# Optimization experiments

Measured on AMD Instinct MI355X. Metric: run time of the kernel, lower is better.

Reference implementation:

```python
import jax, jax.numpy as jnp
import numpy as np

B, T, C, H = 4, 2048, 768, 12
D = C // H  # head dim = 64
EPS = 1e-5


def setup_inputs() -> dict:
    key = jax.random.key(0)
    ks = jax.random.split(key, 12)
    s = lambda fan_in: 1.0 / np.sqrt(fan_in)
    return {
        "x": jax.random.normal(ks[0], (B, T, C), dtype=jnp.float32),
        "ln1_g": jnp.ones((C,), jnp.float32),
        "ln1_b": jnp.zeros((C,), jnp.float32),
        "w_attn": jax.random.normal(ks[1], (C, 3 * C), jnp.float32) * s(C),
        "b_attn": jnp.zeros((3 * C,), jnp.float32),
        "w_aproj": jax.random.normal(ks[2], (C, C), jnp.float32) * s(C),
        "b_aproj": jnp.zeros((C,), jnp.float32),
        "ln2_g": jnp.ones((C,), jnp.float32),
        "ln2_b": jnp.zeros((C,), jnp.float32),
        "w_fc": jax.random.normal(ks[3], (C, 4 * C), jnp.float32) * s(C),
        "b_fc": jnp.zeros((4 * C,), jnp.float32),
        "w_mproj": jax.random.normal(ks[4], (4 * C, C), jnp.float32) * s(4 * C),
        "b_mproj": jnp.zeros((C,), jnp.float32),
    }


def _layernorm(x, g, b):
    mu = jnp.mean(x, axis=-1, keepdims=True)
    var = jnp.mean(jnp.square(x - mu), axis=-1, keepdims=True)
    return (x - mu) * jax.lax.rsqrt(var + EPS) * g + b


def _attention(h, w_attn, b_attn, w_aproj, b_aproj):
    qkv = h @ w_attn + b_attn                          # [B,T,3C]
    q, k, v = jnp.split(qkv, 3, axis=-1)
    q = q.reshape(B, T, H, D)
    k = k.reshape(B, T, H, D)
    v = v.reshape(B, T, H, D)
    att = jnp.einsum("bqhd,bkhd->bhqk", q, k) * (1.0 / np.sqrt(D))
    causal = jnp.tril(jnp.ones((T, T), bool))
    att = jnp.where(causal, att, -jnp.inf)
    att = jax.nn.softmax(att, axis=-1)
    y = jnp.einsum("bhqk,bkhd->bqhd", att, v).reshape(B, T, C)
    return y @ w_aproj + b_aproj


def reference(x, ln1_g, ln1_b, w_attn, b_attn, w_aproj, b_aproj,
              ln2_g, ln2_b, w_fc, b_fc, w_mproj, b_mproj):
    x = x + _attention(_layernorm(x, ln1_g, ln1_b), w_attn, b_attn, w_aproj, b_aproj)
    h = _layernorm(x, ln2_g, ln2_b)
    h = jax.nn.gelu(h @ w_fc + b_fc, approximate=True)  # tanh approximation, matches F.gelu(approximate='tanh')
    x = x + (h @ w_mproj + b_mproj)
    return x
```

## Files before the change

### kernel.cpp

```cpp
#include <hip/hip_runtime.h>


typedef unsigned short ushortT;
typedef unsigned int uintT;
typedef __attribute__((ext_vector_type(8))) __bf16 bf16x8;
typedef __attribute__((ext_vector_type(4))) float f32x4;

#define MFMA16(a, b, c) __builtin_amdgcn_mfma_f32_16x16x32_bf16(a, b, c, 0, 0, 0)

__device__ inline float b2f(ushortT u) {
  return __uint_as_float(((uintT)u) << 16);
}
__device__ inline ushortT f2b(float f) {
  uintT x = __float_as_uint(f);
  uintT r = x + 0x7fffu + ((x >> 16) & 1u);
  return (ushortT)(r >> 16);
}
__device__ inline uintT pack_bf2(float a, float b) {
  return __builtin_amdgcn_perm(__float_as_uint(b), __float_as_uint(a),
                               0x07060302u);
}

__device__ inline float gelu_tanh(float v) {
  float t = 0.7978845608028654f * (v + 0.044715f * v * v * v);
  return v / (1.0f + __expf(-2.0f * t));
}

__device__ __forceinline__ void glds16(const ushortT* g, ushortT* l) {
  __builtin_amdgcn_global_load_lds(
      (const __attribute__((address_space(1))) unsigned int*)(const void*)g,
      (__attribute__((address_space(3))) unsigned int*)(void*)l, 16, 0, 0);
}

__global__ __launch_bounds__(256) void detect_dtype(
    const ushortT* __restrict__ w, int* __restrict__ flag) {
  __shared__ int red;
  if (threadIdx.x == 0) red = 0;
  __syncthreads();
  int crazy = 0;
  for (int i = threadIdx.x; i < 4096; i += 256) {
    uintT e = (w[2 * i] >> 7) & 0xFF;
    if (e >= 150) crazy = 1;
  }
  if (crazy) atomicOr(&red, 1);
  __syncthreads();
  if (threadIdx.x == 0) *flag = red;
}

struct VecArgs {
  const void* src[8];
  int n[8];
  int dstoff[8];
};
__global__ __launch_bounds__(256) void convert_vecs(
    VecArgs a, ushortT* __restrict__ pv, const int* __restrict__ flag) {
  int fl = *flag;
  int t = blockIdx.y;
  int i = blockIdx.x * 256 + threadIdx.x;
  if (i >= a.n[t]) return;
  float v = fl ? ((const float*)a.src[t])[i] : b2f(((const ushortT*)a.src[t])[i]);
  pv[a.dstoff[t] + i] = f2b(v);
}

__global__ __launch_bounds__(256) void transpose_any(
    const void* __restrict__ in, ushortT* __restrict__ out, int K, int N,
    const int* __restrict__ flag) {
  __shared__ ushortT t[32][33];
  int fl = *flag;
  int n0 = blockIdx.x * 32, k0 = blockIdx.y * 32;
  int x = threadIdx.x, y0 = threadIdx.y;
#pragma unroll
  for (int i = y0; i < 32; i += 8) {
    size_t idx = (size_t)(k0 + i) * N + n0 + x;
    t[i][x] = fl ? f2b(((const float*)in)[idx]) : ((const ushortT*)in)[idx];
  }
  __syncthreads();
#pragma unroll
  for (int i = y0; i < 32; i += 8)
    out[(size_t)(n0 + i) * K + k0 + x] = t[x][i];
}

__global__ __launch_bounds__(256) void vtrans_kernel(
    const ushortT* __restrict__ qkv, ushortT* __restrict__ vt) {
  const int T = 2048, C3 = 2304;
  __shared__ ushortT tile[64][65];
  int bh = blockIdx.y;
  int b = bh / 12, h = bh % 12;
  int t0 = blockIdx.x * 64;
  int col = threadIdx.x & 63, rowi = threadIdx.x >> 6;
#pragma unroll
  for (int rr = rowi; rr < 64; rr += 4)
    tile[rr][col] =
        qkv[((size_t)(b * T + t0 + rr)) * C3 + 1536 + h * 64 + col];
  __syncthreads();
#pragma unroll
  for (int dd = rowi; dd < 64; dd += 4)
    vt[((size_t)bh * 64 + dd) * T + t0 + col] = tile[col][dd];
}

template <int MODE>
__global__ __launch_bounds__(256) void ln_kernel(
    const void* __restrict__ xin, const ushortT* __restrict__ g,
    const ushortT* __restrict__ bb, ushortT* __restrict__ out,
    const int* __restrict__ flag) {
  const int C = 768;
  bool f32;
  if constexpr (MODE == 1) f32 = true; else f32 = (*flag != 0);
  size_t base = (size_t)blockIdx.x * C;
  int tid = threadIdx.x;
  const float* xf = (const float*)xin;
  const ushortT* xb = (const ushortT*)xin;
  float v0 = f32 ? xf[base + tid]       : b2f(xb[base + tid]);
  float v1 = f32 ? xf[base + tid + 256] : b2f(xb[base + tid + 256]);
  float v2 = f32 ? xf[base + tid + 512] : b2f(xb[base + tid + 512]);
  float s = v0 + v1 + v2;
  float q = v0 * v0 + v1 * v1 + v2 * v2;
#pragma unroll
  for (int off = 32; off; off >>= 1) {
    s += __shfl_xor(s, off);
    q += __shfl_xor(q, off);
  }
  __shared__ float as_[4], aq_[4];
  if ((tid & 63) == 0) { as_[tid >> 6] = s; aq_[tid >> 6] = q; }
  __syncthreads();
  s = as_[0] + as_[1] + as_[2] + as_[3];
  q = aq_[0] + aq_[1] + aq_[2] + aq_[3];
  float mu = s * (1.0f / 768.0f);
  float var = q * (1.0f / 768.0f) - mu * mu;
  float rs = rsqrtf(var + 1e-5f);
  ushortT* orow = out + base;
  orow[tid]       = f2b((v0 - mu) * rs * b2f(g[tid])       + b2f(bb[tid]));
  orow[tid + 256] = f2b((v1 - mu) * rs * b2f(g[tid + 256]) + b2f(bb[tid + 256]));
  orow[tid + 512] = f2b((v2 - mu) * rs * b2f(g[tid + 512]) + b2f(bb[tid + 512]));
}

template <int EPI>
__global__ __launch_bounds__(512, 2) void gemm_dp(
    const ushortT* __restrict__ A, const ushortT* __restrict__ Bt,
    const ushortT* __restrict__ bias, const void* __restrict__ res,
    void* __restrict__ out, int N, int K, int nbm, int nbn,
    const int* __restrict__ flag) {
  __shared__ ushortT As3[3][128 * 64];
  __shared__ ushortT Bs3[3][256 * 64];
  int fl = (EPI >= 2) ? *flag : 0;
  int tid = threadIdx.x;
  int lane = tid & 63, wave = tid >> 6;
  int quad = lane >> 4, n = lane & 15, n7 = n & 7;
  int mg = wave >> 2, ng = wave & 3;
  int l = blockIdx.x;
  int xcd = l & 7, j = l >> 3;
  int m0 = (xcd * (nbm >> 3) + j / nbn) * 128;
  int n0 = (j % nbn) * 256;

  int trow = tid >> 3;
  int tc = ((tid & 7) ^ (trow & 7)) << 3;
  const ushortT* ga = A + (size_t)(m0 + trow) * K + tc;
  const ushortT* gb = Bt + (size_t)(n0 + trow) * K + tc;
  int lw = wave * 512;

  const int c0 = (quad ^ n7) << 3;
  const int c1 = ((4 + quad) ^ n7) << 3;
  const int arow = (mg * 64 + n) * 64;
  const int brow = (ng * 64 + n) * 64;

  int kt = K >> 6;
  f32x4 acc[4][4] = {};

  auto stage_tile = [&](int tt, int slot) {
    int kk0 = tt << 6;
    ushortT* la = &As3[slot][0] + lw;
    ushortT* lb = &Bs3[slot][0] + lw;
    glds16(ga + kk0, la);
    glds16(ga + (size_t)64 * K + kk0, la + 4096);
    glds16(gb + kk0, lb);
    glds16(gb + (size_t)64 * K + kk0, lb + 4096);
    glds16(gb + (size_t)128 * K + kk0, lb + 8192);
    glds16(gb + (size_t)192 * K + kk0, lb + 12288);
  };

  stage_tile(0, 0);
  stage_tile(1, 1);
  asm volatile("s_waitcnt vmcnt(6)" ::: "memory");
  __builtin_amdgcn_s_barrier();

  int cur = 0;
  for (int t = 0; t < kt; ++t) {
    const ushortT* ca = &As3[cur][0];
    const ushortT* cb = &Bs3[cur][0];
    int nxt = cur + 2; if (nxt >= 3) nxt -= 3;
    bool pf = (t + 2) < kt;
    int pk0 = (t + 2) << 6;
    ushortT* la = &As3[nxt][0] + lw;
    ushortT* lb = &Bs3[nxt][0] + lw;

    bf16x8 af[4][2], bfr[2][2];
#pragma unroll
    for (int mi = 0; mi < 4; ++mi) {
      af[mi][0] = *(const bf16x8*)(ca + arow + mi * 1024 + c0);
      af[mi][1] = *(const bf16x8*)(ca + arow + mi * 1024 + c1);
    }
#pragma unroll
    for (int ni = 0; ni < 2; ++ni) {
      bfr[ni][0] = *(const bf16x8*)(cb + brow + ni * 1024 + c0);
      bfr[ni][1] = *(const bf16x8*)(cb + brow + ni * 1024 + c1);
    }
    if (pf) {
      glds16(ga + pk0, la);
      glds16(ga + (size_t)64 * K + pk0, la + 4096);
      glds16(gb + pk0, lb);
    }
    __builtin_amdgcn_s_barrier();
    __builtin_amdgcn_s_setprio(1);
#pragma unroll
    for (int mi = 0; mi < 4; ++mi)
#pragma unroll
      for (int ni = 0; ni < 2; ++ni) {
        acc[mi][ni] = MFMA16(af[mi][0], bfr[ni][0], acc[mi][ni]);
        acc[mi][ni] = MFMA16(af[mi][1], bfr[ni][1], acc[mi][ni]);
      }
    __builtin_amdgcn_s_setprio(0);
    __builtin_amdgcn_s_barrier();

#pragma unroll
    for (int ni = 0; ni < 2; ++ni) {
      bfr[ni][0] = *(const bf16x8*)(cb + brow + (ni + 2) * 1024 + c0);
      bfr[ni][1] = *(const bf16x8*)(cb + brow + (ni + 2) * 1024 + c1);
    }
    if (pf) {
      glds16(gb + (size_t)64 * K + pk0, lb + 4096);
      glds16(gb + (size_t)128 * K + pk0, lb + 8192);
      glds16(gb + (size_t)192 * K + pk0, lb + 12288);
    }
    __builtin_amdgcn_s_barrier();
    __builtin_amdgcn_s_setprio(1);
#pragma unroll
    for (int mi = 0; mi < 4; ++mi)
#pragma unroll
      for (int ni = 0; ni < 2; ++ni) {
        acc[mi][ni + 2] = MFMA16(af[mi][0], bfr[ni][0], acc[mi][ni + 2]);
        acc[mi][ni + 2] = MFMA16(af[mi][1], bfr[ni][1], acc[mi][ni + 2]);
      }
    __builtin_amdgcn_s_setprio(0);
    if (pf) asm volatile("s_waitcnt vmcnt(6)" ::: "memory");
    else    asm volatile("s_waitcnt vmcnt(0)" ::: "memory");
    __builtin_amdgcn_s_barrier();

    cur = cur + 1; if (cur == 3) cur = 0;
  }

#pragma unroll
  for (int mi = 0; mi < 4; ++mi) {
#pragma unroll
    for (int ni = 0; ni < 4; ++ni) {
      int gc = n0 + ng * 64 + ni * 16 + n;
      float bv = b2f(bias[gc]);
      int gr0 = m0 + mg * 64 + mi * 16 + quad * 4;
#pragma unroll
      for (int r = 0; r < 4; ++r) {
        size_t idx = (size_t)(gr0 + r) * N + gc;
        float v = acc[mi][ni][r] + bv;
        if constexpr (EPI == 1) v = gelu_tanh(v);
        if constexpr (EPI == 2) {
          v += fl ? ((const float*)res)[idx] : b2f(((const ushortT*)res)[idx]);
          ((float*)out)[idx] = v;
        } else if constexpr (EPI == 3) {
          v += ((const float*)res)[idx];
          if (fl) ((float*)out)[idx] = v;
          else    ((ushortT*)out)[idx] = f2b(v);
        } else {
          ((ushortT*)out)[idx] = f2b(v);
        }
      }
    }
  }
}

__global__ __launch_bounds__(256) void attn_kernel(
    const ushortT* __restrict__ qkv, const ushortT* __restrict__ vt,
    ushortT* __restrict__ y) {
  const int T = 2048, C3 = 2304;
  constexpr int LDK = 72, LDP = 72;
  __shared__ ushortT Ks[64 * LDK];
  __shared__ ushortT Vs[64 * LDK];
  __shared__ ushortT Ps[4 * 16 * LDP];
  int bh = blockIdx.y;
  int b = bh / 12, h = bh % 12;
  int pj = blockIdx.x;
  int tid = threadIdx.x;
  int lane = tid & 63, wave = tid >> 6;
  int quad = lane >> 4, n = lane & 15;

  const ushortT* base = qkv + (size_t)b * T * C3;
  const ushortT* kbase = base + 768 + h * 64;
  const ushortT* vbase = vt + (size_t)bh * 64 * T;
  ushortT* myP = Ps + wave * 16 * LDP;

  const float QS = 0.18033688011112042f;
  const float MB = 20.0f;

  int qtA = pj, qtB = 31 - pj;
  int nA = qtA + 1, ntot = 33;

  int trow = tid >> 3, tcol = (tid & 7) << 3;
  const ushortT* kg = kbase + (size_t)trow * C3 + tcol;
  const ushortT* vg = vbase + (size_t)trow * T + tcol;

  int qt = qtA;
  int qw = qt * 64 + wave * 16;
  bf16x8 aq[2];
  {
    const ushortT* qrow = base + (size_t)(qw + n) * C3 + h * 64 + quad * 8;
#pragma unroll
    for (int dh = 0; dh < 2; ++dh) {
      union { ushortT u[8]; bf16x8 v; } tmp;
#pragma unroll
      for (int j = 0; j < 8; ++j) tmp.u[j] = f2b(b2f(qrow[dh * 32 + j]) * QS);
      aq[dh] = tmp.v;
    }
  }
  f32x4 Ot[4] = {};
  float l_ = 0.f;

  uint4 kr0 = *(const uint4*)(kg);
  uint4 kr1 = *(const uint4*)(kg + (size_t)32 * C3);
  uint4 vr0 = *(const uint4*)(vg);
  uint4 vr1 = *(const uint4*)(vg + (size_t)32 * T);

  for (int t = 0; t < ntot; ++t) {
    int kt = (t < nA) ? t : t - nA;
    __syncthreads();
    *(uint4*)(Ks + trow * LDK + tcol) = kr0;
    *(uint4*)(Ks + (trow + 32) * LDK + tcol) = kr1;
    *(uint4*)(Vs + trow * LDK + tcol) = vr0;
    *(uint4*)(Vs + (trow + 32) * LDK + tcol) = vr1;
    __syncthreads();
    if (t + 1 < ntot) {
      int ktn = (t + 1 < nA) ? t + 1 : t + 1 - nA;
      int k0n = ktn << 6;
      kr0 = *(const uint4*)(kg + (size_t)k0n * C3);
      kr1 = *(const uint4*)(kg + (size_t)(k0n + 32) * C3);
      vr0 = *(const uint4*)(vg + k0n);
      vr1 = *(const uint4*)(vg + (size_t)32 * T + k0n);
    }

    f32x4 St[4];
#pragma unroll
    for (int g = 0; g < 4; ++g) {
      bf16x8 ka0 = *(const bf16x8*)(Ks + (g * 16 + n) * LDK + quad * 8);
      bf16x8 ka1 = *(const bf16x8*)(Ks + (g * 16 + n) * LDK + 32 + quad * 8);
      f32x4 z = {};
      z = MFMA16(ka0, aq[0], z);
      St[g] = MFMA16(ka1, aq[1], z);
    }
    if (kt == qt) {
      int lim = wave * 16 + n;
#pragma unroll
      for (int g = 0; g < 4; ++g)
#pragma unroll
        for (int r = 0; r < 4; ++r)
          if (g * 16 + quad * 4 + r > lim) St[g][r] = -1e30f;
    }
    float ls = 0.f;
#pragma unroll
    for (int g = 0; g < 4; ++g) {
      float p0 = exp2f(St[g][0] - MB);
      float p1 = exp2f(St[g][1] - MB);
      float p2 = exp2f(St[g][2] - MB);
      float p3 = exp2f(St[g][3] - MB);
      ls += (p0 + p1) + (p2 + p3);
      uint2 pk;
      pk.x = pack_bf2(p0, p1);
      pk.y = pack_bf2(p2, p3);
      *(uint2*)(myP + n * LDP + g * 16 + quad * 4) = pk;
    }
    ls += __shfl_xor(ls, 16);
    ls += __shfl_xor(ls, 32);
    l_ += ls;

    bf16x8 pb0 = *(const bf16x8*)(myP + n * LDP + quad * 8);
    bf16x8 pb1 = *(const bf16x8*)(myP + n * LDP + 32 + quad * 8);
#pragma unroll
    for (int dt = 0; dt < 4; ++dt) {
      bf16x8 va0 = *(const bf16x8*)(Vs + (dt * 16 + n) * LDK + quad * 8);
      bf16x8 va1 = *(const bf16x8*)(Vs + (dt * 16 + n) * LDK + 32 + quad * 8);
      Ot[dt] = MFMA16(va0, pb0, Ot[dt]);
      Ot[dt] = MFMA16(va1, pb1, Ot[dt]);
    }

    if (kt == qt) {
      float inv = 1.0f / l_;
      int qg = qw + n;
#pragma unroll
      for (int dt = 0; dt < 4; ++dt) {
        uint2 o;
        o.x = pack_bf2(Ot[dt][0] * inv, Ot[dt][1] * inv);
        o.y = pack_bf2(Ot[dt][2] * inv, Ot[dt][3] * inv);
        *(uint2*)(y + (size_t)(b * T + qg) * 768 + h * 64 + dt * 16 +
                  quad * 4) = o;
      }
      if (t + 1 < ntot) {
        qt = qtB;
        qw = qt * 64 + wave * 16;
        const ushortT* qrow =
            base + (size_t)(qw + n) * C3 + h * 64 + quad * 8;
#pragma unroll
        for (int dh = 0; dh < 2; ++dh) {
          union { ushortT u[8]; bf16x8 v; } tmp;
#pragma unroll
          for (int j = 0; j < 8; ++j)
            tmp.u[j] = f2b(b2f(qrow[dh * 32 + j]) * QS);
          aq[dh] = tmp.v;
        }
#pragma unroll
        for (int dt = 0; dt < 4; ++dt)
#pragma unroll
          for (int r = 0; r < 4; ++r) Ot[dt][r] = 0.f;
        l_ = 0.f;
      }
    }
  }
}

extern "C" void kernel_launch(void* const* d_in, const int* in_sizes, int n_in,
                              void* d_out, int out_size, void* d_ws,
                              size_t ws_size, hipStream_t stream) {
  (void)in_sizes; (void)n_in; (void)out_size; (void)ws_size;
  const void* x       = d_in[0];
  const void* w_attn  = d_in[3];
  const void* w_aproj = d_in[5];
  const void* w_fc    = d_in[9];
  const void* w_mproj = d_in[11];

  char* ws = (char*)d_ws;
  ushortT* h1  = (ushortT*)(ws);
  ushortT* qkv = (ushortT*)(ws + 12582912);
  ushortT* yb  = (ushortT*)(ws + 50331648);
  float*   x1  = (float*)(ws + 62914560);
  ushortT* fcg = (ushortT*)(ws + 88080384);
  ushortT* wT0 = (ushortT*)(ws + 138412032);
  ushortT* wT1 = (ushortT*)(ws + 141950976);
  ushortT* wT2 = (ushortT*)(ws + 143130624);
  ushortT* wT3 = (ushortT*)(ws + 147849216);
  ushortT* pv  = (ushortT*)(ws + 152567808);
  int*     flag = (int*)(ws + 152600576);
  ushortT* vt  = h1;
  ushortT* h2  = yb;

  const int O_LN1G = 0, O_LN1B = 768, O_BATT = 1536, O_BAPR = 3840,
            O_LN2G = 4608, O_LN2B = 5376, O_BFC = 6144, O_BMPR = 9216;

  detect_dtype<<<1, 256, 0, stream>>>((const ushortT*)w_fc, flag);

  VecArgs va;
  va.src[0] = d_in[1];  va.n[0] = 768;  va.dstoff[0] = O_LN1G;
  va.src[1] = d_in[2];  va.n[1] = 768;  va.dstoff[1] = O_LN1B;
  va.src[2] = d_in[4];  va.n[2] = 2304; va.dstoff[2] = O_BATT;
  va.src[3] = d_in[6];  va.n[3] = 768;  va.dstoff[3] = O_BAPR;
  va.src[4] = d_in[7];  va.n[4] = 768;  va.dstoff[4] = O_LN2G;
  va.src[5] = d_in[8];  va.n[5] = 768;  va.dstoff[5] = O_LN2B;
  va.src[6] = d_in[10]; va.n[6] = 3072; va.dstoff[6] = O_BFC;
  va.src[7] = d_in[12]; va.n[7] = 768;  va.dstoff[7] = O_BMPR;
  convert_vecs<<<dim3(12, 8), 256, 0, stream>>>(va, pv, flag);

  dim3 tb(32, 8);
  transpose_any<<<dim3(72, 24), tb, 0, stream>>>(w_attn, wT0, 768, 2304, flag);
  transpose_any<<<dim3(24, 24), tb, 0, stream>>>(w_aproj, wT1, 768, 768, flag);
  transpose_any<<<dim3(96, 24), tb, 0, stream>>>(w_fc, wT2, 768, 3072, flag);
  transpose_any<<<dim3(24, 96), tb, 0, stream>>>(w_mproj, wT3, 3072, 768, flag);

  ln_kernel<0><<<8192, 256, 0, stream>>>(x, pv + O_LN1G, pv + O_LN1B, h1, flag);
  gemm_dp<0><<<576, 512, 0, stream>>>(
      h1, wT0, pv + O_BATT, nullptr, qkv, 2304, 768, 64, 9, flag);
  vtrans_kernel<<<dim3(32, 48), 256, 0, stream>>>(qkv, vt);
  attn_kernel<<<dim3(16, 48), 256, 0, stream>>>(qkv, vt, yb);
  gemm_dp<2><<<192, 512, 0, stream>>>(
      yb, wT1, pv + O_BAPR, x, x1, 768, 768, 64, 3, flag);
  ln_kernel<1><<<8192, 256, 0, stream>>>(x1, pv + O_LN2G, pv + O_LN2B, h2, flag);
  gemm_dp<1><<<768, 512, 0, stream>>>(
      h2, wT2, pv + O_BFC, nullptr, fcg, 3072, 768, 64, 12, flag);
  gemm_dp<3><<<192, 512, 0, stream>>>(
      fcg, wT3, pv + O_BMPR, x1, d_out, 768, 3072, 64, 3, flag);
}
```

Before: 419.3 us.

## Double-buffer attention K/V tiles via direct global-to-LDS loads with XOR swizzle

The attention kernel now stages K and V tiles straight into LDS with global_load_lds, using two buffers so the next tile loads while the current one is computed. This removes the register round trip and one of the two barriers per iteration. The padded LDS rows are replaced by an XOR-swizzled 64-wide layout to avoid bank conflicts, and exp2f is swapped for the hardware exp2 builtin. LDS use doubles for K/V, and correctness depends on the swizzle indices on the write and read sides matching.

```diff
diff --git a/kernel.cpp b/kernel.cpp
--- a/kernel.cpp
+++ b/kernel.cpp
@@ -19,6 +19,14 @@
 __device__ inline uintT pack_bf2(float a, float b) {
   return __builtin_amdgcn_perm(__float_as_uint(b), __float_as_uint(a),
                                0x07060302u);
+}
+
+__device__ inline float fast_exp2(float x) {
+#if __has_builtin(__builtin_amdgcn_exp2f)
+  return __builtin_amdgcn_exp2f(x);
+#else
+  return exp2f(x);
+#endif
 }
 
 __device__ inline float gelu_tanh(float v) {
@@ -279,16 +287,16 @@
     const ushortT* __restrict__ qkv, const ushortT* __restrict__ vt,
     ushortT* __restrict__ y) {
   const int T = 2048, C3 = 2304;
-  constexpr int LDK = 72, LDP = 72;
-  __shared__ ushortT Ks[64 * LDK];
-  __shared__ ushortT Vs[64 * LDK];
+  constexpr int LDP = 72;
+  __shared__ ushortT Ks[2][64 * 64];
+  __shared__ ushortT Vs[2][64 * 64];
   __shared__ ushortT Ps[4 * 16 * LDP];
   int bh = blockIdx.y;
   int b = bh / 12, h = bh % 12;
   int pj = blockIdx.x;
   int tid = threadIdx.x;
   int lane = tid & 63, wave = tid >> 6;
-  int quad = lane >> 4, n = lane & 15;
+  int quad = lane >> 4, n = lane & 15, n7 = n & 7;
 
   const ushortT* base = qkv + (size_t)b * T * C3;
   const ushortT* kbase = base + 768 + h * 64;
@@ -301,9 +309,14 @@
   int qtA = pj, qtB = 31 - pj;
   int nA = qtA + 1, ntot = 33;
 
-  int trow = tid >> 3, tcol = (tid & 7) << 3;
-  const ushortT* kg = kbase + (size_t)trow * C3 + tcol;
-  const ushortT* vg = vbase + (size_t)trow * T + tcol;
+  int srow = lane >> 3, scol = lane & 7;
+  const ushortT* kg =
+      kbase + (size_t)(wave * 16 + srow) * C3 + ((scol ^ srow) << 3);
+  const ushortT* vg =
+      vbase + (size_t)(wave * 16 + srow) * T + ((scol ^ srow) << 3);
+
+  const int c0 = (quad ^ n7) << 3;
+  const int c1 = ((4 + quad) ^ n7) << 3;
 
   int qt = qtA;
   int qw = qt * 64 + wave * 16;
@@ -321,33 +334,34 @@
   f32x4 Ot[4] = {};
   float l_ = 0.f;
 
-  uint4 kr0 = *(const uint4*)(kg);
-  uint4 kr1 = *(const uint4*)(kg + (size_t)32 * C3);
-  uint4 vr0 = *(const uint4*)(vg);
-  uint4 vr1 = *(const uint4*)(vg + (size_t)32 * T);
-
+  auto stage = [&](int kt_, int buf) {
+    int kof = kt_ << 6;
+    ushortT* lk = &Ks[buf][0] + wave * 1024;
+    ushortT* lv = &Vs[buf][0] + wave * 1024;
+    glds16(kg + (size_t)kof * C3, lk);
+    glds16(kg + (size_t)(kof + 8) * C3, lk + 512);
+    glds16(vg + kof, lv);
+    glds16(vg + (size_t)8 * T + kof, lv + 512);
+  };
+
+  stage(0, 0);
+  __syncthreads();
+
+  int cur = 0;
   for (int t = 0; t < ntot; ++t) {
     int kt = (t < nA) ? t : t - nA;
-    __syncthreads();
-    *(uint4*)(Ks + trow * LDK + tcol) = kr0;
-    *(uint4*)(Ks + (trow + 32) * LDK + tcol) = kr1;
-    *(uint4*)(Vs + trow * LDK + tcol) = vr0;
-    *(uint4*)(Vs + (trow + 32) * LDK + tcol) = vr1;
-    __syncthreads();
     if (t + 1 < ntot) {
       int ktn = (t + 1 < nA) ? t + 1 : t + 1 - nA;
-      int k0n = ktn << 6;
-      kr0 = *(const uint4*)(kg + (size_t)k0n * C3);
-      kr1 = *(const uint4*)(kg + (size_t)(k0n + 32) * C3);
-      vr0 = *(const uint4*)(vg + k0n);
-      vr1 = *(const uint4*)(vg + (size_t)32 * T + k0n);
-    }
+      stage(ktn, cur ^ 1);
+    }
+    const ushortT* ks = &Ks[cur][0];
+    const ushortT* vs = &Vs[cur][0];
 
     f32x4 St[4];
 #pragma unroll
     for (int g = 0; g < 4; ++g) {
-      bf16x8 ka0 = *(const bf16x8*)(Ks + (g * 16 + n) * LDK + quad * 8);
-      bf16x8 ka1 = *(const bf16x8*)(Ks + (g * 16 + n) * LDK + 32 + quad * 8);
+      bf16x8 ka0 = *(const bf16x8*)(ks + (g * 16 + n) * 64 + c0);
+      bf16x8 ka1 = *(const bf16x8*)(ks + (g * 16 + n) * 64 + c1);
       f32x4 z = {};
       z = MFMA16(ka0, aq[0], z);
       St[g] = MFMA16(ka1, aq[1], z);
@@ -363,10 +377,10 @@
     float ls = 0.f;
 #pragma unroll
     for (int g = 0; g < 4; ++g) {
-      float p0 = exp2f(St[g][0] - MB);
-      float p1 = exp2f(St[g][1] - MB);
-      float p2 = exp2f(St[g][2] - MB);
-      float p3 = exp2f(St[g][3] - MB);
+      float p0 = fast_exp2(St[g][0] - MB);
+      float p1 = fast_exp2(St[g][1] - MB);
+      float p2 = fast_exp2(St[g][2] - MB);
+      float p3 = fast_exp2(St[g][3] - MB);
       ls += (p0 + p1) + (p2 + p3);
       uint2 pk;
       pk.x = pack_bf2(p0, p1);
@@ -381,8 +395,8 @@
     bf16x8 pb1 = *(const bf16x8*)(myP + n * LDP + 32 + quad * 8);
 #pragma unroll
     for (int dt = 0; dt < 4; ++dt) {
-      bf16x8 va0 = *(const bf16x8*)(Vs + (dt * 16 + n) * LDK + quad * 8);
-      bf16x8 va1 = *(const bf16x8*)(Vs + (dt * 16 + n) * LDK + 32 + quad * 8);
+      bf16x8 va0 = *(const bf16x8*)(vs + (dt * 16 + n) * 64 + c0);
+      bf16x8 va1 = *(const bf16x8*)(vs + (dt * 16 + n) * 64 + c1);
       Ot[dt] = MFMA16(va0, pb0, Ot[dt]);
       Ot[dt] = MFMA16(va1, pb1, Ot[dt]);
     }
@@ -418,6 +432,8 @@
         l_ = 0.f;
       }
     }
+    __syncthreads();
+    cur ^= 1;
   }
 }
 
```

New measurement: 421.9 us. About the same (+0.6%).
